# Kernel tuning notes

Measured on AMD Instinct MI355X. Metric: run time of the kernel, lower is better.

## Reference

```python
import jax, jax.numpy as jnp
import numpy as np

QK_DIM = 64
V_DIM = 64
NUM_Q_HEADS = 16
NUM_KV_HEADS = 4
GROUP = NUM_Q_HEADS // NUM_KV_HEADS
SCALE = 1.0 / (QK_DIM ** 0.5)


def setup_inputs() -> dict:
    key = jax.random.key(0)
    kq, kk, kv = jax.random.split(key, 3)
    B, S = 2, 2048
    Q = jax.random.normal(kq, (B, S, NUM_Q_HEADS * QK_DIM), dtype=jnp.float32)
    K = jax.random.normal(kk, (B, S, NUM_KV_HEADS * QK_DIM), dtype=jnp.float32)
    V = jax.random.normal(kv, (B, S, NUM_KV_HEADS * V_DIM), dtype=jnp.float32)
    # causal mask, [B, 1, S, S]; 0 entries are masked (matches masked_fill(mask == 0, -inf))
    mask = jnp.broadcast_to(jnp.tril(jnp.ones((S, S), dtype=jnp.int32))[None, None], (B, 1, S, S))
    return {"Q": Q, "K": K, "V": V, "mask": mask}


def reference(Q, K, V, mask):
    B, S, _ = Q.shape
    # [B, Hkv, g, S, d]
    Qg = Q.reshape(B, S, NUM_Q_HEADS, QK_DIM).transpose(0, 2, 1, 3).reshape(B, NUM_KV_HEADS, GROUP, S, QK_DIM)
    Kh = K.reshape(B, S, NUM_KV_HEADS, QK_DIM).transpose(0, 2, 1, 3)  # [B, Hkv, S, d]
    Vh = V.reshape(B, S, NUM_KV_HEADS, V_DIM).transpose(0, 2, 1, 3)   # [B, Hkv, S, dv]
    # scores: [B, Hkv, g, S, S]
    scores = jnp.einsum('bhgsd,bhtd->bhgst', Qg, Kh) * SCALE
    scores = jnp.where(mask[:, None] == 0, -jnp.inf, scores)
    probs = jax.nn.softmax(scores, axis=-1)
    # dropout p=0.0 -> identity (eval semantics)
    out = jnp.einsum('bhgst,bhtv->bhgsv', probs, Vh)
    return out
```

## Files before the change

kernel.cpp:

```cpp
#include <hip/hip_runtime.h>
#include <hip/hip_bf16.h>

typedef unsigned short u16;
typedef unsigned int u32;
typedef __attribute__((ext_vector_type(8))) short bf16x8;
typedef __attribute__((ext_vector_type(4))) float f32x4;

#define S_LEN 2048
#define NHQ   16
#define NHKV  4
#define HD    64
#define KVBLK 64
#define QBLK  128
#define LPAD  72
#define QSCALE 0.18033688011112042f
#define DEFER_THR 8.0f

__device__ __forceinline__ u32 cvt2(float lo, float hi) {
    __hip_bfloat162 h = __float22bfloat162_rn(make_float2(lo, hi));
    union { __hip_bfloat162 h; u32 u; } c; c.h = h; return c.u;
}
__device__ __forceinline__ u16 cvt1(float x) {
    __hip_bfloat16 h = __float2bfloat16(x);
    union { __hip_bfloat16 h; u16 u; } c; c.h = h; return c.u;
}

__global__ __launch_bounds__(512, 2)
void gqa_fwd_kernel(const float* __restrict__ Qp, const float* __restrict__ Kp,
                    const float* __restrict__ Vp, float* __restrict__ Op)
{
    __shared__ __align__(16) u16 Kl[2][KVBLK][LPAD];
    __shared__ __align__(16) u16 Vt[2][HD][LPAD];
    __shared__ __align__(16) u16 Pl[8][16][LPAD];

    const int tid  = threadIdx.x;
    const int w    = tid >> 6;
    const int lane = tid & 63;
    const int l16  = lane & 15;
    const int quad = lane >> 4;

    const int bid = blockIdx.x;
    const int kvh = bid & 3;
    const int b   = (bid >> 2) & 1;
    const int j   = (bid >> 3) & 7;
    const int g   = bid >> 6;
    const int qh  = kvh * 4 + g;

    const float* Kbase = Kp + (size_t)b * S_LEN * (NHKV*HD) + kvh*HD;
    const float* Vbase = Vp + (size_t)b * S_LEN * (NHKV*HD) + kvh*HD;
    const float* Qhead = Qp + (size_t)b * S_LEN * (NHQ*HD) + qh*HD;
    float*       Ohead = Op + (size_t)(b*NHQ + qh) * S_LEN * HD;

    const int krow = tid >> 4;
    const int kc4  = (tid & 15) * 4;
    const int vrow = tid & 63;
    const int vc0  = w * 4;

    const int relq = (w << 4) + l16;
    const int rk0w = (w >> 2) << 6;
    int cur = 0;

    #pragma unroll 1
    for (int pass = 0; pass < 2; ++pass) {
        const int qt = pass ? j : (15 - j);
        const int q0 = qt * QBLK;
        const int nt = 2*qt + 1;
        const int tlast = 2*qt + (w >> 2);

        bf16x8 qf[2];
        {
            const float* qp = Qhead + (size_t)(q0 + relq) * (NHQ*HD);
            #pragma unroll
            for (int kk = 0; kk < 2; ++kk) {
                const float4 x = *(const float4*)(qp + kk*32 + quad*8);
                const float4 y = *(const float4*)(qp + kk*32 + quad*8 + 4);
                u32 tmp[4];
                tmp[0] = cvt2(x.x*QSCALE, x.y*QSCALE);
                tmp[1] = cvt2(x.z*QSCALE, x.w*QSCALE);
                tmp[2] = cvt2(y.x*QSCALE, y.y*QSCALE);
                tmp[3] = cvt2(y.z*QSCALE, y.w*QSCALE);
                qf[kk] = *(bf16x8*)tmp;
            }
        }

        f32x4 oacc[4];
        #pragma unroll
        for (int nb = 0; nb < 4; ++nb) { oacc[nb][0]=0.f; oacc[nb][1]=0.f; oacc[nb][2]=0.f; oacc[nb][3]=0.f; }
        float m_s = -1e30f;
        float l_p = 0.f;

        const float* kpt = Kbase + (size_t)(KVBLK + krow)*(NHKV*HD) + kc4;
        const float* vpt = Vbase + (size_t)(KVBLK + vrow)*(NHKV*HD) + vc0;

        __syncthreads();
        {
            const float* kp0 = Kbase + (size_t)krow*(NHKV*HD) + kc4;
            const float* vp0 = Vbase + (size_t)vrow*(NHKV*HD) + vc0;
            #pragma unroll
            for (int i = 0; i < 2; ++i) {
                const float4 kx = *(const float4*)(kp0 + (size_t)(32*i)*(NHKV*HD));
                *(uint2*)(&Kl[cur][krow + 32*i][kc4]) = make_uint2(cvt2(kx.x,kx.y), cvt2(kx.z,kx.w));
                const float4 vx = *(const float4*)(vp0 + 32*i);
                Vt[cur][vc0+32*i+0][vrow] = cvt1(vx.x);
                Vt[cur][vc0+32*i+1][vrow] = cvt1(vx.y);
                Vt[cur][vc0+32*i+2][vrow] = cvt1(vx.z);
                Vt[cur][vc0+32*i+3][vrow] = cvt1(vx.w);
            }
        }
        __syncthreads();

        for (int t = 0; t <= nt; ++t) {
            const bool pf_on = (t < nt);

            float4 kpf[2], vpf[2];
            if (pf_on) {
                #pragma unroll
                for (int i = 0; i < 2; ++i) {
                    kpf[i] = *(const float4*)(kpt + (size_t)(32*i)*(NHKV*HD));
                    vpf[i] = *(const float4*)(vpt + 32*i);
                }
            }

            if (t <= tlast) {
                f32x4 s[4];
                __builtin_amdgcn_s_setprio(1);
                #pragma unroll
                for (int nb = 0; nb < 4; ++nb) {
                    f32x4 acc = {0.f,0.f,0.f,0.f};
                    #pragma unroll
                    for (int kk = 0; kk < 2; ++kk) {
                        bf16x8 kf = *(const bf16x8*)(&Kl[cur][nb*16 + l16][kk*32 + quad*8]);
                        acc = __builtin_amdgcn_mfma_f32_16x16x32_bf16(kf, qf[kk], acc, 0, 0, 0);
                    }
                    s[nb] = acc;
                }
                __builtin_amdgcn_s_setprio(0);

                if (t == tlast) {
                    #pragma unroll
                    for (int nb = 0; nb < 4; ++nb)
                        #pragma unroll
                        for (int r = 0; r < 4; ++r)
                            if (rk0w + nb*16 + quad*4 + r > relq) s[nb][r] = -1e30f;
                }

                float a0 = fmaxf(fmaxf(s[0][0], s[0][1]), fmaxf(s[0][2], s[0][3]));
                float a1 = fmaxf(fmaxf(s[1][0], s[1][1]), fmaxf(s[1][2], s[1][3]));
                float a2 = fmaxf(fmaxf(s[2][0], s[2][1]), fmaxf(s[2][2], s[2][3]));
                float a3 = fmaxf(fmaxf(s[3][0], s[3][1]), fmaxf(s[3][2], s[3][3]));
                const float lmax = fmaxf(fmaxf(a0, a1), fmaxf(a2, a3));

                if (!__all(lmax <= m_s + DEFER_THR)) {
                    float rmax = fmaxf(lmax, __shfl_xor(lmax, 16));
                    rmax = fmaxf(rmax, __shfl_xor(rmax, 32));
                    const float mnew = fmaxf(m_s, rmax);
                    const float cf   = __builtin_amdgcn_exp2f(m_s - mnew);
                    m_s = mnew;
                    l_p *= cf;
                    #pragma unroll
                    for (int nb = 0; nb < 4; ++nb)
                        #pragma unroll
                        for (int r = 0; r < 4; ++r) oacc[nb][r] *= cf;
                }

                float ps[4];
                #pragma unroll
                for (int nb = 0; nb < 4; ++nb) {
                    const float p0 = __builtin_amdgcn_exp2f(s[nb][0] - m_s);
                    const float p1 = __builtin_amdgcn_exp2f(s[nb][1] - m_s);
                    const float p2 = __builtin_amdgcn_exp2f(s[nb][2] - m_s);
                    const float p3 = __builtin_amdgcn_exp2f(s[nb][3] - m_s);
                    s[nb][0]=p0; s[nb][1]=p1; s[nb][2]=p2; s[nb][3]=p3;
                    ps[nb] = (p0 + p1) + (p2 + p3);
                }
                l_p += (ps[0] + ps[1]) + (ps[2] + ps[3]);

                #pragma unroll
                for (int nb = 0; nb < 4; ++nb)
                    *(uint2*)(&Pl[w][l16][nb*16 + quad*4]) =
                        make_uint2(cvt2(s[nb][0], s[nb][1]), cvt2(s[nb][2], s[nb][3]));
                bf16x8 pfrag[2];
                #pragma unroll
                for (int kk = 0; kk < 2; ++kk)
                    pfrag[kk] = *(const bf16x8*)(&Pl[w][l16][kk*32 + quad*8]);

                __builtin_amdgcn_s_setprio(1);
                #pragma unroll
                for (int nb = 0; nb < 4; ++nb) {
                    #pragma unroll
                    for (int kk = 0; kk < 2; ++kk) {
                        bf16x8 vf = *(const bf16x8*)(&Vt[cur][nb*16 + l16][kk*32 + quad*8]);
                        oacc[nb] = __builtin_amdgcn_mfma_f32_16x16x32_bf16(vf, pfrag[kk], oacc[nb], 0, 0, 0);
                    }
                }
                __builtin_amdgcn_s_setprio(0);
            }

            if (pf_on) {
                #pragma unroll
                for (int i = 0; i < 2; ++i) {
                    *(uint2*)(&Kl[cur^1][krow + 32*i][kc4]) =
                        make_uint2(cvt2(kpf[i].x,kpf[i].y), cvt2(kpf[i].z,kpf[i].w));
                    Vt[cur^1][vc0+32*i+0][vrow] = cvt1(vpf[i].x);
                    Vt[cur^1][vc0+32*i+1][vrow] = cvt1(vpf[i].y);
                    Vt[cur^1][vc0+32*i+2][vrow] = cvt1(vpf[i].z);
                    Vt[cur^1][vc0+32*i+3][vrow] = cvt1(vpf[i].w);
                }
                kpt += KVBLK * (NHKV*HD);
                vpt += KVBLK * (NHKV*HD);
                __syncthreads();
                cur ^= 1;
            }
        }

        l_p += __shfl_xor(l_p, 16);
        l_p += __shfl_xor(l_p, 32);
        const float inv = 1.0f / l_p;

        float* ob = Ohead + (size_t)(q0 + relq) * HD;
        #pragma unroll
        for (int nb = 0; nb < 4; ++nb) {
            float4 o4;
            o4.x = oacc[nb][0] * inv;
            o4.y = oacc[nb][1] * inv;
            o4.z = oacc[nb][2] * inv;
            o4.w = oacc[nb][3] * inv;
            *(float4*)(ob + nb*16 + quad*4) = o4;
        }
    }
}

extern "C" void kernel_launch(void* const* d_in, const int* in_sizes, int n_in,
                              void* d_out, int out_size, void* d_ws, size_t ws_size,
                              hipStream_t stream) {
    const float* Q = (const float*)d_in[0];
    const float* K = (const float*)d_in[1];
    const float* V = (const float*)d_in[2];
    float* O = (float*)d_out;
    gqa_fwd_kernel<<<dim3(256), dim3(512), 0, stream>>>(Q, K, V, O);
}
```

Baseline: 47.15 us.

## Split work into 64-row query tiles with 256-thread blocks and heavy-first ordering

```diff
diff --git a/kernel.cpp b/kernel.cpp
--- a/kernel.cpp
+++ b/kernel.cpp
@@ -11,27 +11,28 @@
 #define NHKV  4
 #define HD    64
 #define KVBLK 64
-#define QBLK  128
 #define LPAD  72
+#define KVSTR (NHKV*HD)
+#define QSTR  (NHQ*HD)
 #define QSCALE 0.18033688011112042f
 #define DEFER_THR 8.0f
 
 __device__ __forceinline__ u32 cvt2(float lo, float hi) {
-    __hip_bfloat162 h = __float22bfloat162_rn(make_float2(lo, hi));
-    union { __hip_bfloat162 h; u32 u; } c; c.h = h; return c.u;
+    __hip_bfloat162 hh = __float22bfloat162_rn(make_float2(lo, hi));
+    union { __hip_bfloat162 h; u32 u; } c; c.h = hh; return c.u;
 }
 __device__ __forceinline__ u16 cvt1(float x) {
-    __hip_bfloat16 h = __float2bfloat16(x);
-    union { __hip_bfloat16 h; u16 u; } c; c.h = h; return c.u;
-}
-
-__global__ __launch_bounds__(512, 2)
+    __hip_bfloat16 hh = __float2bfloat16(x);
+    union { __hip_bfloat16 h; u16 u; } c; c.h = hh; return c.u;
+}
+
+__global__ __launch_bounds__(256, 3)
 void gqa_fwd_kernel(const float* __restrict__ Qp, const float* __restrict__ Kp,
                     const float* __restrict__ Vp, float* __restrict__ Op)
 {
     __shared__ __align__(16) u16 Kl[2][KVBLK][LPAD];
     __shared__ __align__(16) u16 Vt[2][HD][LPAD];
-    __shared__ __align__(16) u16 Pl[8][16][LPAD];
+    __shared__ __align__(16) u16 Pl[4][16][LPAD];
 
     const int tid  = threadIdx.x;
     const int w    = tid >> 6;
@@ -39,194 +40,174 @@
     const int l16  = lane & 15;
     const int quad = lane >> 4;
 
-    const int bid = blockIdx.x;
-    const int kvh = bid & 3;
-    const int b   = (bid >> 2) & 1;
-    const int j   = (bid >> 3) & 7;
-    const int g   = bid >> 6;
-    const int qh  = kvh * 4 + g;
-
-    const float* Kbase = Kp + (size_t)b * S_LEN * (NHKV*HD) + kvh*HD;
-    const float* Vbase = Vp + (size_t)b * S_LEN * (NHKV*HD) + kvh*HD;
-    const float* Qhead = Qp + (size_t)b * S_LEN * (NHQ*HD) + qh*HD;
-    float*       Ohead = Op + (size_t)(b*NHQ + qh) * S_LEN * HD;
-
-    const int krow = tid >> 4;
-    const int kc4  = (tid & 15) * 4;
+    const int bid  = blockIdx.x;
+    const int head = bid & 31;
+    const int g    = bid >> 5;
+    const int gi   = g & 7;
+    const int gs   = g >> 3;
+    const int qt   = (gs == 0) ? (31 - gi) : (gs == 1) ? (16 + gi)
+                   : (gs == 2) ? (15 - gi) : gi;
+    const int kvh  = head & 3;
+    const int b    = (head >> 2) & 1;
+    const int qh   = kvh * 4 + (head >> 3);
+
+    const int relq = w * 16 + l16;
+    const int qrow = qt * 64 + relq;
+
+    const float* Kbase = Kp + (size_t)b * S_LEN * KVSTR + kvh*HD;
+    const float* Vbase = Vp + (size_t)b * S_LEN * KVSTR + kvh*HD;
+    const float* qp    = Qp + ((size_t)b * S_LEN + qrow) * QSTR + qh*HD;
+    float*       ob    = Op + ((size_t)(b*NHQ + qh) * S_LEN + qrow) * HD;
+
+    const int krow = tid >> 2;
+    const int kd   = (tid & 3) * 16;
     const int vrow = tid & 63;
-    const int vc0  = w * 4;
-
-    const int relq = (w << 4) + l16;
-    const int rk0w = (w >> 2) << 6;
-    int cur = 0;
-
-    #pragma unroll 1
-    for (int pass = 0; pass < 2; ++pass) {
-        const int qt = pass ? j : (15 - j);
-        const int q0 = qt * QBLK;
-        const int nt = 2*qt + 1;
-        const int tlast = 2*qt + (w >> 2);
-
-        bf16x8 qf[2];
-        {
-            const float* qp = Qhead + (size_t)(q0 + relq) * (NHQ*HD);
+    const int vd0  = w * 16;
+
+    float4 kpf[4], vpf[4];
+
+    auto ISSUE = [&](int tt) {
+        const float* kp = Kbase + (size_t)(tt*KVBLK + krow)*KVSTR + kd;
+        const float* vp = Vbase + (size_t)(tt*KVBLK + vrow)*KVSTR + vd0;
+        #pragma unroll
+        for (int ii = 0; ii < 4; ++ii) {
+            kpf[ii] = *(const float4*)(kp + 4*ii);
+            vpf[ii] = *(const float4*)(vp + 4*ii);
+        }
+        asm volatile("" ::: "memory");
+    };
+    auto WRITE = [&](int bf) {
+        *(uint4*)(&Kl[bf][krow][kd]) = make_uint4(
+            cvt2(kpf[0].x,kpf[0].y), cvt2(kpf[0].z,kpf[0].w),
+            cvt2(kpf[1].x,kpf[1].y), cvt2(kpf[1].z,kpf[1].w));
+        *(uint4*)(&Kl[bf][krow][kd+8]) = make_uint4(
+            cvt2(kpf[2].x,kpf[2].y), cvt2(kpf[2].z,kpf[2].w),
+            cvt2(kpf[3].x,kpf[3].y), cvt2(kpf[3].z,kpf[3].w));
+        #pragma unroll
+        for (int ii = 0; ii < 4; ++ii) {
+            Vt[bf][vd0+4*ii+0][vrow] = cvt1(vpf[ii].x);
+            Vt[bf][vd0+4*ii+1][vrow] = cvt1(vpf[ii].y);
+            Vt[bf][vd0+4*ii+2][vrow] = cvt1(vpf[ii].z);
+            Vt[bf][vd0+4*ii+3][vrow] = cvt1(vpf[ii].w);
+        }
+    };
+
+    bf16x8 qf[2];
+    #pragma unroll
+    for (int kk = 0; kk < 2; ++kk) {
+        const float4 x = *(const float4*)(qp + kk*32 + quad*8);
+        const float4 y = *(const float4*)(qp + kk*32 + quad*8 + 4);
+        union { u32 u[4]; bf16x8 v; } t4;
+        t4.u[0] = cvt2(x.x*QSCALE, x.y*QSCALE);
+        t4.u[1] = cvt2(x.z*QSCALE, x.w*QSCALE);
+        t4.u[2] = cvt2(y.x*QSCALE, y.y*QSCALE);
+        t4.u[3] = cvt2(y.z*QSCALE, y.w*QSCALE);
+        qf[kk] = t4.v;
+    }
+
+    f32x4 oacc[4];
+    #pragma unroll
+    for (int nb = 0; nb < 4; ++nb) { oacc[nb][0]=0.f; oacc[nb][1]=0.f; oacc[nb][2]=0.f; oacc[nb][3]=0.f; }
+    float m_s = -1e30f;
+    float l_p = 0.f;
+
+    ISSUE(0);
+    WRITE(0);
+    __syncthreads();
+
+    for (int t = 0; t <= qt; ++t) {
+        const bool pf_on = (t < qt);
+        if (pf_on) ISSUE(t + 1);
+
+        const int bf = t & 1;
+        f32x4 s[4];
+        __builtin_amdgcn_s_setprio(1);
+        #pragma unroll
+        for (int nb = 0; nb < 4; ++nb) {
+            f32x4 acc = {0.f,0.f,0.f,0.f};
             #pragma unroll
             for (int kk = 0; kk < 2; ++kk) {
-                const float4 x = *(const float4*)(qp + kk*32 + quad*8);
-                const float4 y = *(const float4*)(qp + kk*32 + quad*8 + 4);
-                u32 tmp[4];
-                tmp[0] = cvt2(x.x*QSCALE, x.y*QSCALE);
-                tmp[1] = cvt2(x.z*QSCALE, x.w*QSCALE);
-                tmp[2] = cvt2(y.x*QSCALE, y.y*QSCALE);
-                tmp[3] = cvt2(y.z*QSCALE, y.w*QSCALE);
-                qf[kk] = *(bf16x8*)tmp;
+                bf16x8 kf = *(const bf16x8*)(&Kl[bf][nb*16 + l16][kk*32 + quad*8]);
+                acc = __builtin_amdgcn_mfma_f32_16x16x32_bf16(kf, qf[kk], acc, 0, 0, 0);
             }
-        }
-
-        f32x4 oacc[4];
-        #pragma unroll
-        for (int nb = 0; nb < 4; ++nb) { oacc[nb][0]=0.f; oacc[nb][1]=0.f; oacc[nb][2]=0.f; oacc[nb][3]=0.f; }
-        float m_s = -1e30f;
-        float l_p = 0.f;
-
-        const float* kpt = Kbase + (size_t)(KVBLK + krow)*(NHKV*HD) + kc4;
-        const float* vpt = Vbase + (size_t)(KVBLK + vrow)*(NHKV*HD) + vc0;
-
+            s[nb] = acc;
+        }
+        __builtin_amdgcn_s_setprio(0);
+
+        if (t == qt) {
+            #pragma unroll
+            for (int nb = 0; nb < 4; ++nb)
+                #pragma unroll
+                for (int r = 0; r < 4; ++r)
+                    if (nb*16 + quad*4 + r > relq) s[nb][r] = -1e30f;
+        }
+
+        float a0 = fmaxf(fmaxf(s[0][0], s[0][1]), fmaxf(s[0][2], s[0][3]));
+        float a1 = fmaxf(fmaxf(s[1][0], s[1][1]), fmaxf(s[1][2], s[1][3]));
+        float a2 = fmaxf(fmaxf(s[2][0], s[2][1]), fmaxf(s[2][2], s[2][3]));
+        float a3 = fmaxf(fmaxf(s[3][0], s[3][1]), fmaxf(s[3][2], s[3][3]));
+        const float lmax = fmaxf(fmaxf(a0, a1), fmaxf(a2, a3));
+
+        if (!__all(lmax <= m_s + DEFER_THR)) {
+            float rmax = fmaxf(lmax, __shfl_xor(lmax, 16));
+            rmax = fmaxf(rmax, __shfl_xor(rmax, 32));
+            const float mnew = fmaxf(m_s, rmax);
+            const float cf   = __builtin_amdgcn_exp2f(m_s - mnew);
+            m_s = mnew;
+            l_p *= cf;
+            #pragma unroll
+            for (int nb = 0; nb < 4; ++nb)
+                #pragma unroll
+                for (int r = 0; r < 4; ++r) oacc[nb][r] *= cf;
+        }
+
+        float ps[4];
+        #pragma unroll
+        for (int nb = 0; nb < 4; ++nb) {
+            const float p0 = __builtin_amdgcn_exp2f(s[nb][0] - m_s);
+            const float p1 = __builtin_amdgcn_exp2f(s[nb][1] - m_s);
+            const float p2 = __builtin_amdgcn_exp2f(s[nb][2] - m_s);
+            const float p3 = __builtin_amdgcn_exp2f(s[nb][3] - m_s);
+            s[nb][0]=p0; s[nb][1]=p1; s[nb][2]=p2; s[nb][3]=p3;
+            ps[nb] = (p0 + p1) + (p2 + p3);
+        }
+        l_p += (ps[0] + ps[1]) + (ps[2] + ps[3]);
+
+        #pragma unroll
+        for (int nb = 0; nb < 4; ++nb)
+            *(uint2*)(&Pl[w][l16][nb*16 + quad*4]) =
+                make_uint2(cvt2(s[nb][0], s[nb][1]), cvt2(s[nb][2], s[nb][3]));
+        bf16x8 pfrag[2];
+        #pragma unroll
+        for (int kk = 0; kk < 2; ++kk)
+            pfrag[kk] = *(const bf16x8*)(&Pl[w][l16][kk*32 + quad*8]);
+
+        __builtin_amdgcn_s_setprio(1);
+        #pragma unroll
+        for (int nb = 0; nb < 4; ++nb) {
+            #pragma unroll
+            for (int kk = 0; kk < 2; ++kk) {
+                bf16x8 vf = *(const bf16x8*)(&Vt[bf][nb*16 + l16][kk*32 + quad*8]);
+                oacc[nb] = __builtin_amdgcn_mfma_f32_16x16x32_bf16(vf, pfrag[kk], oacc[nb], 0, 0, 0);
+            }
+        }
+        __builtin_amdgcn_s_setprio(0);
+
+        if (pf_on) WRITE(bf ^ 1);
         __syncthreads();
-        {
-            const float* kp0 = Kbase + (size_t)krow*(NHKV*HD) + kc4;
-            const float* vp0 = Vbase + (size_t)vrow*(NHKV*HD) + vc0;
-            #pragma unroll
-            for (int i = 0; i < 2; ++i) {
-                const float4 kx = *(const float4*)(kp0 + (size_t)(32*i)*(NHKV*HD));
-                *(uint2*)(&Kl[cur][krow + 32*i][kc4]) = make_uint2(cvt2(kx.x,kx.y), cvt2(kx.z,kx.w));
-                const float4 vx = *(const float4*)(vp0 + 32*i);
-                Vt[cur][vc0+32*i+0][vrow] = cvt1(vx.x);
-                Vt[cur][vc0+32*i+1][vrow] = cvt1(vx.y);
-                Vt[cur][vc0+32*i+2][vrow] = cvt1(vx.z);
-                Vt[cur][vc0+32*i+3][vrow] = cvt1(vx.w);
-            }
-        }
-        __syncthreads();
-
-        for (int t = 0; t <= nt; ++t) {
-            const bool pf_on = (t < nt);
-
-            float4 kpf[2], vpf[2];
-            if (pf_on) {
-                #pragma unroll
-                for (int i = 0; i < 2; ++i) {
-                    kpf[i] = *(const float4*)(kpt + (size_t)(32*i)*(NHKV*HD));
-                    vpf[i] = *(const float4*)(vpt + 32*i);
-                }
-            }
-
-            if (t <= tlast) {
-                f32x4 s[4];
-                __builtin_amdgcn_s_setprio(1);
-                #pragma unroll
-                for (int nb = 0; nb < 4; ++nb) {
-                    f32x4 acc = {0.f,0.f,0.f,0.f};
-                    #pragma unroll
-                    for (int kk = 0; kk < 2; ++kk) {
-                        bf16x8 kf = *(const bf16x8*)(&Kl[cur][nb*16 + l16][kk*32 + quad*8]);
-                        acc = __builtin_amdgcn_mfma_f32_16x16x32_bf16(kf, qf[kk], acc, 0, 0, 0);
-                    }
-                    s[nb] = acc;
-                }
-                __builtin_amdgcn_s_setprio(0);
-
-                if (t == tlast) {
-                    #pragma unroll
-                    for (int nb = 0; nb < 4; ++nb)
-                        #pragma unroll
-                        for (int r = 0; r < 4; ++r)
-                            if (rk0w + nb*16 + quad*4 + r > relq) s[nb][r] = -1e30f;
-                }
-
-                float a0 = fmaxf(fmaxf(s[0][0], s[0][1]), fmaxf(s[0][2], s[0][3]));
-                float a1 = fmaxf(fmaxf(s[1][0], s[1][1]), fmaxf(s[1][2], s[1][3]));
-                float a2 = fmaxf(fmaxf(s[2][0], s[2][1]), fmaxf(s[2][2], s[2][3]));
-                float a3 = fmaxf(fmaxf(s[3][0], s[3][1]), fmaxf(s[3][2], s[3][3]));
-                const float lmax = fmaxf(fmaxf(a0, a1), fmaxf(a2, a3));
-
-                if (!__all(lmax <= m_s + DEFER_THR)) {
-                    float rmax = fmaxf(lmax, __shfl_xor(lmax, 16));
-                    rmax = fmaxf(rmax, __shfl_xor(rmax, 32));
-                    const float mnew = fmaxf(m_s, rmax);
-                    const float cf   = __builtin_amdgcn_exp2f(m_s - mnew);
-                    m_s = mnew;
-                    l_p *= cf;
-                    #pragma unroll
-                    for (int nb = 0; nb < 4; ++nb)
-                        #pragma unroll
-                        for (int r = 0; r < 4; ++r) oacc[nb][r] *= cf;
-                }
-
-                float ps[4];
-                #pragma unroll
-                for (int nb = 0; nb < 4; ++nb) {
-                    const float p0 = __builtin_amdgcn_exp2f(s[nb][0] - m_s);
-                    const float p1 = __builtin_amdgcn_exp2f(s[nb][1] - m_s);
-                    const float p2 = __builtin_amdgcn_exp2f(s[nb][2] - m_s);
-                    const float p3 = __builtin_amdgcn_exp2f(s[nb][3] - m_s);
-                    s[nb][0]=p0; s[nb][1]=p1; s[nb][2]=p2; s[nb][3]=p3;
-                    ps[nb] = (p0 + p1) + (p2 + p3);
-                }
-                l_p += (ps[0] + ps[1]) + (ps[2] + ps[3]);
-
-                #pragma unroll
-                for (int nb = 0; nb < 4; ++nb)
-                    *(uint2*)(&Pl[w][l16][nb*16 + quad*4]) =
-                        make_uint2(cvt2(s[nb][0], s[nb][1]), cvt2(s[nb][2], s[nb][3]));
-                bf16x8 pfrag[2];
-                #pragma unroll
-                for (int kk = 0; kk < 2; ++kk)
-                    pfrag[kk] = *(const bf16x8*)(&Pl[w][l16][kk*32 + quad*8]);
-
-                __builtin_amdgcn_s_setprio(1);
-                #pragma unroll
-                for (int nb = 0; nb < 4; ++nb) {
-                    #pragma unroll
-                    for (int kk = 0; kk < 2; ++kk) {
-                        bf16x8 vf = *(const bf16x8*)(&Vt[cur][nb*16 + l16][kk*32 + quad*8]);
-                        oacc[nb] = __builtin_amdgcn_mfma_f32_16x16x32_bf16(vf, pfrag[kk], oacc[nb], 0, 0, 0);
-                    }
-                }
-                __builtin_amdgcn_s_setprio(0);
-            }
-
-            if (pf_on) {
-                #pragma unroll
-                for (int i = 0; i < 2; ++i) {
-                    *(uint2*)(&Kl[cur^1][krow + 32*i][kc4]) =
-                        make_uint2(cvt2(kpf[i].x,kpf[i].y), cvt2(kpf[i].z,kpf[i].w));
-                    Vt[cur^1][vc0+32*i+0][vrow] = cvt1(vpf[i].x);
-                    Vt[cur^1][vc0+32*i+1][vrow] = cvt1(vpf[i].y);
-                    Vt[cur^1][vc0+32*i+2][vrow] = cvt1(vpf[i].z);
-                    Vt[cur^1][vc0+32*i+3][vrow] = cvt1(vpf[i].w);
-                }
-                kpt += KVBLK * (NHKV*HD);
-                vpt += KVBLK * (NHKV*HD);
-                __syncthreads();
-                cur ^= 1;
-            }
-        }
-
-        l_p += __shfl_xor(l_p, 16);
-        l_p += __shfl_xor(l_p, 32);
-        const float inv = 1.0f / l_p;
-
-        float* ob = Ohead + (size_t)(q0 + relq) * HD;
-        #pragma unroll
-        for (int nb = 0; nb < 4; ++nb) {
-            float4 o4;
-            o4.x = oacc[nb][0] * inv;
-            o4.y = oacc[nb][1] * inv;
-            o4.z = oacc[nb][2] * inv;
-            o4.w = oacc[nb][3] * inv;
-            *(float4*)(ob + nb*16 + quad*4) = o4;
-        }
+    }
+
+    l_p += __shfl_xor(l_p, 16);
+    l_p += __shfl_xor(l_p, 32);
+    const float inv = 1.0f / l_p;
+    #pragma unroll
+    for (int nb = 0; nb < 4; ++nb) {
+        float4 o4;
+        o4.x = oacc[nb][0] * inv;
+        o4.y = oacc[nb][1] * inv;
+        o4.z = oacc[nb][2] * inv;
+        o4.w = oacc[nb][3] * inv;
+        *(float4*)(ob + nb*16 + quad*4) = o4;
     }
 }
 
@@ -237,5 +218,5 @@
     const float* K = (const float*)d_in[1];
     const float* V = (const float*)d_in[2];
     float* O = (float*)d_out;
-    gqa_fwd_kernel<<<dim3(256), dim3(512), 0, stream>>>(Q, K, V, O);
-}
+    gqa_fwd_kernel<<<dim3(1024), dim3(256), 0, stream>>>(Q, K, V, O);
+}
```

Result: slower. 63.17 us (+34.0%).
